# Kernel optimization log

Hardware: AMD Instinct MI355X
Metric: run time of the kernel (lower is better)

## Reference

```python
import jax, jax.numpy as jnp
import numpy as np
import math

IMG, P, C, D, DEPTH, H, MLP, NCLS, B = 224, 16, 3, 768, 12, 12, 3072, 1000, 32
G = IMG // P          # 14 patches per side
N = G * G             # 196 patches
S = N + 1             # 197 tokens (cls + patches)
DK = D // H
PD = P * P * C        # 768 flattened patch dim


def layer_norm(x, g, b, eps=1e-5):
    mu = jnp.mean(x, axis=-1, keepdims=True)
    var = jnp.mean((x - mu) ** 2, axis=-1, keepdims=True)
    return (x - mu) * jax.lax.rsqrt(var + eps) * g + b


def setup_inputs() -> dict:
    key = jax.random.key(0)
    ks = iter(jax.random.split(key, 32))
    nrm = lambda shape, s=0.02: jax.random.normal(next(ks), shape, jnp.float32) * s
    inp = {
        'x': jax.random.normal(next(ks), (B, C, IMG, IMG), jnp.float32),
        'patch_W': nrm((PD, D)), 'patch_b': jnp.zeros((D,)),
        'cls_token': nrm((1, 1, D)), 'pos_embed': nrm((1, S, D)),
        'Wq': nrm((DEPTH, D, D)), 'bq': jnp.zeros((DEPTH, D)),
        'Wk': nrm((DEPTH, D, D)), 'bk': jnp.zeros((DEPTH, D)),
        'Wv': nrm((DEPTH, D, D)), 'bv': jnp.zeros((DEPTH, D)),
        'Wo': nrm((DEPTH, D, D)), 'bo': jnp.zeros((DEPTH, D)),
        'ln1_g': jnp.ones((DEPTH, D)), 'ln1_b': jnp.zeros((DEPTH, D)),
        'ln2_g': jnp.ones((DEPTH, D)), 'ln2_b': jnp.zeros((DEPTH, D)),
        'W1': nrm((DEPTH, D, MLP)), 'b1': jnp.zeros((DEPTH, MLP)),
        'W2': nrm((DEPTH, MLP, D)), 'b2': jnp.zeros((DEPTH, D)),
        'lnp_g': jnp.ones((D,)), 'lnp_b': jnp.zeros((D,)),
        'head_W': nrm((D, NCLS)), 'head_b': jnp.zeros((NCLS,)),
    }
    return inp


def vit_forward(x, patch_W, patch_b, cls_token, pos_embed,
                Wq, bq, Wk, bk, Wv, bv, Wo, bo,
                ln1_g, ln1_b, ln2_g, ln2_b, W1, b1, W2, b2,
                lnp_g, lnp_b, head_W, head_b):
    b = x.shape[0]
    # faithful replication of torch unfold(2).unfold(3).view: (B,C,G,P,G,P)->(B,C,G,G,P,P)->row-major flatten
    patches = x.reshape(b, C, G, P, G, P).transpose(0, 1, 2, 4, 3, 5).reshape(b, N, PD)
    h = patches @ patch_W + patch_b                              # [B,N,D]
    h = jnp.concatenate([jnp.broadcast_to(cls_token, (b, 1, D)), h], axis=1) + pos_embed
    scale = 1.0 / math.sqrt(DK)
    for i in range(DEPTH):
        y = layer_norm(h, ln1_g[i], ln1_b[i])
        q = (y @ Wq[i] + bq[i]).reshape(b, S, H, DK).transpose(0, 2, 1, 3)
        k = (y @ Wk[i] + bk[i]).reshape(b, S, H, DK).transpose(0, 2, 1, 3)
        v = (y @ Wv[i] + bv[i]).reshape(b, S, H, DK).transpose(0, 2, 1, 3)
        attn = jax.nn.softmax(jnp.einsum('bhqd,bhkd->bhqk', q, k) * scale, axis=-1)
        att = jnp.einsum('bhqk,bhkd->bhqd', attn, v).transpose(0, 2, 1, 3).reshape(b, S, D)
        h = h + att @ Wo[i] + bo[i]
        y = layer_norm(h, ln2_g[i], ln2_b[i])
        h = h + jax.nn.gelu(y @ W1[i] + b1[i], approximate=False) @ W2[i] + b2[i]
    h = layer_norm(h, lnp_g, lnp_b)
    return h[:, 0] @ head_W + head_b                              # [B, NCLS]


def reference(x, patch_W, patch_b, cls_token, pos_embed,
              Wq, bq, Wk, bk, Wv, bv, Wo, bo,
              ln1_g, ln1_b, ln2_g, ln2_b, W1, b1, W2, b2,
              lnp_g, lnp_b, head_W, head_b):
    return vit_forward(x, patch_W, patch_b, cls_token, pos_embed,
                       Wq, bq, Wk, bk, Wv, bv, Wo, bo,
                       ln1_g, ln1_b, ln2_g, ln2_b, W1, b1, W2, b2,
                       lnp_g, lnp_b, head_W, head_b)
```

## Files before the change

kernel.cpp:

```cpp
#include <hip/hip_runtime.h>
#include <hip/hip_bf16.h>


typedef __attribute__((ext_vector_type(8))) short short8;
typedef __attribute__((ext_vector_type(4))) float f32x4;
typedef __attribute__((ext_vector_type(4))) unsigned short us4;

#define MFMA16(a, b, c) __builtin_amdgcn_mfma_f32_16x16x32_bf16(a, b, c, 0, 0, 0)

#define BATCH 32
#define SEQ 197
#define SPAD 208
#define DIM 768
#define HEADS 12
#define DKH 64
#define MLPD 3072
#define NCLS 1000
#define NPATCH 196
#define PDIM 768
#define QKVD 2304
#define ROWS (BATCH * SPAD)

static __device__ __forceinline__ unsigned short f2bf(float f) {
    unsigned int u = __builtin_bit_cast(unsigned int, f);
    u += 0x7fffu + ((u >> 16) & 1u);
    return (unsigned short)(u >> 16);
}

__device__ __forceinline__ void gload16(const void* g, void* l) {
    __builtin_amdgcn_global_load_lds(
        (const __attribute__((address_space(1))) void*)g,
        (__attribute__((address_space(3))) void*)l, 16, 0, 0);
}

__global__ __launch_bounds__(256) void patchify(const float* __restrict__ x,
                                                unsigned short* __restrict__ out) {
    int i = blockIdx.x * 256 + threadIdx.x;
    if (i >= BATCH * NPATCH * PDIM) return;
    int b = i / (NPATCH * PDIM);
    int f = i % (NPATCH * PDIM);
    int c = f / 50176, r = f % 50176;
    int gy = r / 3584, r2 = r % 3584;
    int gx = r2 >> 8, r3 = r2 & 255;
    int py = r3 >> 4, px = r3 & 15;
    float v = x[(((size_t)b * 3 + c) * 224 + gy * 16 + py) * 224 + gx * 16 + px];
    out[i] = f2bf(v);
}

__global__ __launch_bounds__(256) void embed_misc(const float* __restrict__ cls,
                                                  const float* __restrict__ pos,
                                                  float* __restrict__ h) {
    int b = blockIdx.x, t = threadIdx.x;
    float* hb = h + (size_t)b * SPAD * DIM;
    for (int d = t; d < DIM; d += 256) hb[d] = cls[d] + pos[d];
    for (int i = t; i < (SPAD - SEQ) * DIM; i += 256) hb[SEQ * DIM + i] = 0.f;
}

__global__ __launch_bounds__(256) void tconv(const float* __restrict__ src,
                                             unsigned short* __restrict__ dst,
                                             int K, int N) {
    __shared__ float tile[32][33];
    int tn = blockIdx.x, tk = blockIdx.y;
    int t = threadIdx.x, r = t >> 3, c4 = (t & 7) << 2;
    float4 v = *reinterpret_cast<const float4*>(&src[(size_t)(tk * 32 + r) * N + tn * 32 + c4]);
    tile[r][c4 + 0] = v.x; tile[r][c4 + 1] = v.y;
    tile[r][c4 + 2] = v.z; tile[r][c4 + 3] = v.w;
    __syncthreads();
    us4 o = { f2bf(tile[c4 + 0][r]), f2bf(tile[c4 + 1][r]),
              f2bf(tile[c4 + 2][r]), f2bf(tile[c4 + 3][r]) };
    *reinterpret_cast<us4*>(&dst[(size_t)(tn * 32 + r) * K + tk * 32 + c4]) = o;
}

__global__ __launch_bounds__(256) void hconv(const float* __restrict__ src,
                                             unsigned short* __restrict__ dst) {
    __shared__ float tile[32][33];
    int tn = blockIdx.x, tk = blockIdx.y;
    int t = threadIdx.x, r = t >> 3, c4 = (t & 7) << 2;
#pragma unroll
    for (int i = 0; i < 4; ++i) {
        int c = tn * 32 + c4 + i;
        tile[r][c4 + i] = (c < NCLS) ? src[(size_t)(tk * 32 + r) * NCLS + c] : 0.f;
    }
    __syncthreads();
    us4 o = { f2bf(tile[c4 + 0][r]), f2bf(tile[c4 + 1][r]),
              f2bf(tile[c4 + 2][r]), f2bf(tile[c4 + 3][r]) };
    *reinterpret_cast<us4*>(&dst[(size_t)(tn * 32 + r) * 768 + tk * 32 + c4]) = o;
}

__global__ __launch_bounds__(256) void wconvert(const float* __restrict__ q,
                                                const float* __restrict__ k,
                                                const float* __restrict__ v,
                                                const float* __restrict__ o,
                                                const float* __restrict__ w1,
                                                const float* __restrict__ w2,
                                                unsigned short* __restrict__ wT) {
    __shared__ float tile[32][33];
    int tb = blockIdx.x;
    const float* src; unsigned short* dst; int K, N;
    if (tb < 2304) {
        K = 768; N = 768;
        int m = tb / 576; tb -= m * 576;
        src = (m == 0) ? q : (m == 1) ? k : (m == 2) ? v : o;
        dst = wT + (m < 3 ? (size_t)m * 589824 : (size_t)1769472);
    } else if (tb < 4608) {
        tb -= 2304; K = 768; N = 3072; src = w1; dst = wT + 2359296;
    } else {
        tb -= 4608; K = 3072; N = 768; src = w2; dst = wT + 4718592;
    }
    int TN = N >> 5;
    int tn = tb % TN, tk = tb / TN;
    int t = threadIdx.x, r = t >> 3, c4 = (t & 7) << 2;
    float4 vv = *reinterpret_cast<const float4*>(&src[(size_t)(tk * 32 + r) * N + tn * 32 + c4]);
    tile[r][c4 + 0] = vv.x; tile[r][c4 + 1] = vv.y;
    tile[r][c4 + 2] = vv.z; tile[r][c4 + 3] = vv.w;
    __syncthreads();
    us4 ov = { f2bf(tile[c4 + 0][r]), f2bf(tile[c4 + 1][r]),
               f2bf(tile[c4 + 2][r]), f2bf(tile[c4 + 3][r]) };
    *reinterpret_cast<us4*>(&dst[(size_t)(tn * 32 + r) * K + tk * 32 + c4]) = ov;
}

__global__ __launch_bounds__(256) void pack_bias(const float* __restrict__ bq,
                                                 const float* __restrict__ bk,
                                                 const float* __restrict__ bv,
                                                 float* __restrict__ dst) {
    int i = blockIdx.x * 256 + threadIdx.x;
    if (i >= 12 * QKVD) return;
    int l = i / QKVD, c = i % QKVD;
    float v = (c < 768) ? bq[l * 768 + c]
            : (c < 1536) ? bk[l * 768 + c - 768]
                         : bv[l * 768 + c - 1536];
    dst[i] = v;
}

#define MM1(MF, J, NF) \
    acc[MF][NF] = MFMA16(af[J][0], bfr[NF][0], acc[MF][NF]); \
    acc[MF][NF] = MFMA16(af[J][1], bfr[NF][1], acc[MF][NF]);
#define MMROW(MF, J) MM1(MF, J, 0) MM1(MF, J, 1) MM1(MF, J, 2) MM1(MF, J, 3)

#define WAITVM(N) \
    __builtin_amdgcn_sched_barrier(0); \
    asm volatile("s_waitcnt vmcnt(" #N ")" ::: "memory"); \
    __builtin_amdgcn_sched_barrier(0);

template <int MODE>
__global__ __launch_bounds__(512, 2) void gemm8p(
    const unsigned short* __restrict__ A, const unsigned short* __restrict__ Bt,
    const float* __restrict__ bias, int N, int K,
    unsigned short* __restrict__ outb) {
    __shared__ unsigned short Ab[2][16384];
    __shared__ unsigned short Bb[2][16384];
    const int tid = threadIdx.x, lane = tid & 63, wid = tid >> 6;
    const int wm = wid >> 2, wn = wid & 3;
    const int lr = lane & 15, lg = lane >> 4;
    const int ric = lane >> 3, sswz = (lane & 7) ^ ric;
    const int row0 = blockIdx.x * 256, col0 = blockIdx.y * 256;
    const char* pA = (const char*)A + ((size_t)(row0 + wid * 8 + ric) * K) * 2 + sswz * 16;
    const char* pB = (const char*)Bt + ((size_t)(col0 + wid * 8 + ric) * K) * 2 + sswz * 16;
    const int NT = K >> 6;

    auto stA = [&](int q, int ks, int b) {
        gload16(pA + ((size_t)q * 64 * K + ks) * 2, (char*)&Ab[b][0] + q * 8192 + wid * 1024);
    };
    auto stB = [&](int q, int ks, int b) {
        gload16(pB + ((size_t)q * 64 * K + ks) * 2, (char*)&Bb[b][0] + q * 8192 + wid * 1024);
    };

    f32x4 acc[8][4];
#pragma unroll
    for (int m = 0; m < 8; ++m)
#pragma unroll
        for (int n = 0; n < 4; ++n) acc[m][n] = (f32x4){0.f, 0.f, 0.f, 0.f};

    stB(0, 0, 0); stB(1, 0, 0); stB(2, 0, 0); stB(3, 0, 0);
    stA(0, 0, 0); stA(2, 0, 0); stA(1, 0, 0); stA(3, 0, 0);
    if (NT > 1) {
        stB(0, 64, 1); stB(1, 64, 1); stB(2, 64, 1); stB(3, 64, 1);
        stA(0, 64, 1); stA(2, 64, 1);
        WAITVM(4)
    } else {
        WAITVM(0)
    }
    __builtin_amdgcn_s_barrier();

    const int rsw = lr & 7;
    for (int s = 0; s < NT; ++s) {
        const int d = s & 1;
        const unsigned short* Ad = &Ab[d][0];
        const unsigned short* Bd = &Bb[d][0];
        const bool p1ok = (s + 1 < NT), p2ok = (s + 2 < NT);
        short8 bfr[4][2], af[2][2];
#pragma unroll
        for (int nf = 0; nf < 4; ++nf)
#pragma unroll
            for (int kk = 0; kk < 2; ++kk)
                bfr[nf][kk] = *reinterpret_cast<const short8*>(
                    &Bd[(wn * 64 + nf * 16 + lr) * 64 + (((kk * 4 + lg) ^ rsw) << 3)]);
#pragma unroll
        for (int j = 0; j < 2; ++j)
#pragma unroll
            for (int kk = 0; kk < 2; ++kk)
                af[j][kk] = *reinterpret_cast<const short8*>(
                    &Ad[(wm * 128 + (0 + j) * 16 + lr) * 64 + (((kk * 4 + lg) ^ rsw) << 3)]);
        if (p1ok) { stA(1, (s + 1) * 64, d ^ 1); stA(3, (s + 1) * 64, d ^ 1); }
        __builtin_amdgcn_s_barrier();
        __builtin_amdgcn_s_setprio(1);
        MMROW(0, 0) MMROW(1, 1)
        __builtin_amdgcn_s_setprio(0);
        __builtin_amdgcn_s_barrier();
#pragma unroll
        for (int j = 0; j < 2; ++j)
#pragma unroll
            for (int kk = 0; kk < 2; ++kk)
                af[j][kk] = *reinterpret_cast<const short8*>(
                    &Ad[(wm * 128 + (2 + j) * 16 + lr) * 64 + (((kk * 4 + lg) ^ rsw) << 3)]);
        if (p2ok) { stB(0, (s + 2) * 64, d); stB(1, (s + 2) * 64, d); }
        __builtin_amdgcn_s_barrier();
        __builtin_amdgcn_s_setprio(1);
        MMROW(2, 0) MMROW(3, 1)
        __builtin_amdgcn_s_setprio(0);
        __builtin_amdgcn_s_barrier();
#pragma unroll
        for (int j = 0; j < 2; ++j)
#pragma unroll
            for (int kk = 0; kk < 2; ++kk)
                af[j][kk] = *reinterpret_cast<const short8*>(
                    &Ad[(wm * 128 + (4 + j) * 16 + lr) * 64 + (((kk * 4 + lg) ^ rsw) << 3)]);
        if (p2ok) { stB(2, (s + 2) * 64, d); stB(3, (s + 2) * 64, d); }
        __builtin_amdgcn_s_barrier();
        __builtin_amdgcn_s_setprio(1);
        MMROW(4, 0) MMROW(5, 1)
        __builtin_amdgcn_s_setprio(0);
        __builtin_amdgcn_s_barrier();
#pragma unroll
        for (int j = 0; j < 2; ++j)
#pragma unroll
            for (int kk = 0; kk < 2; ++kk)
                af[j][kk] = *reinterpret_cast<const short8*>(
                    &Ad[(wm * 128 + (6 + j) * 16 + lr) * 64 + (((kk * 4 + lg) ^ rsw) << 3)]);
        if (p2ok) {
            stA(0, (s + 2) * 64, d); stA(2, (s + 2) * 64, d);
            WAITVM(4)
        } else {
            WAITVM(0)
        }
        __builtin_amdgcn_s_barrier();
        __builtin_amdgcn_s_setprio(1);
        MMROW(6, 0) MMROW(7, 1)
        __builtin_amdgcn_s_setprio(0);
        __builtin_amdgcn_s_barrier();
    }
#pragma unroll
    for (int m = 0; m < 8; ++m) {
#pragma unroll
        for (int n = 0; n < 4; ++n) {
            int gcol = col0 + wn * 64 + n * 16 + lr;
            float bv = bias[gcol];
#pragma unroll
            for (int i = 0; i < 4; ++i) {
                int grow = row0 + wm * 128 + m * 16 + lg * 4 + i;
                float v = acc[m][n][i] + bv;
                if (MODE == 2) v = 0.5f * v * (1.f + erff(v * 0.70710678118654752f));
                outb[(size_t)grow * N + gcol] = f2bf(v);
            }
        }
    }
}

template <int BM>
__global__ __launch_bounds__(256) void gemm_tn(
    const unsigned short* __restrict__ A, const unsigned short* __restrict__ Bt,
    const float* __restrict__ bias, int M, int N, int K, int mode,
    unsigned short* __restrict__ outb, float* __restrict__ outf,
    const float* __restrict__ pos) {
    constexpr int MFRAG = BM / 32;
    constexpr int ACH = BM / 8;
    constexpr int TOT = ACH + 16;
    constexpr int CPW = TOT / 4;
    __shared__ unsigned short Alds[BM * 64];
    __shared__ unsigned short Blds[128 * 64];
    const int tid = threadIdx.x, lane = tid & 63, wid = tid >> 6;
    const int row0 = blockIdx.x * BM, col0 = blockIdx.y * 128;
    const int wm = (wid >> 1) * (BM / 2), wn = (wid & 1) * 64;
    const int lr = lane & 15, lg = lane >> 4;
    const int ric = lane >> 3;
    const int sswz = (lane & 7) ^ ric;

    const char* gptr[CPW];
    char* lptr[CPW];
#pragma unroll
    for (int j = 0; j < CPW; ++j) {
        int cc = wid * CPW + j;
        if (cc < ACH) {
            int grow = row0 + cc * 8 + ric;
            gptr[j] = (const char*)A + (size_t)grow * K * 2 + sswz * 16;
            lptr[j] = (char*)Alds + cc * 1024;
        } else {
            int grow = col0 + (cc - ACH) * 8 + ric;
            gptr[j] = (const char*)Bt + (size_t)grow * K * 2 + sswz * 16;
            lptr[j] = (char*)Blds + (cc - ACH) * 1024;
        }
    }

    f32x4 acc[MFRAG][4];
#pragma unroll
    for (int m = 0; m < MFRAG; ++m)
#pragma unroll
        for (int n = 0; n < 4; ++n) acc[m][n] = (f32x4){0.f, 0.f, 0.f, 0.f};

    const int rsw = lr & 7;
    for (int ks = 0; ks < K; ks += 64) {
        __syncthreads();
#pragma unroll
        for (int j = 0; j < CPW; ++j) {
            gload16(gptr[j], lptr[j]);
            gptr[j] += 128;
        }
        __syncthreads();
        short8 af[MFRAG][2], bfr[4][2];
#pragma unroll
        for (int m = 0; m < MFRAG; ++m)
#pragma unroll
            for (int kk = 0; kk < 2; ++kk)
                af[m][kk] = *reinterpret_cast<const short8*>(
                    &Alds[(wm + m * 16 + lr) * 64 + (((kk * 4 + lg) ^ rsw) << 3)]);
#pragma unroll
        for (int n = 0; n < 4; ++n)
#pragma unroll
            for (int kk = 0; kk < 2; ++kk)
                bfr[n][kk] = *reinterpret_cast<const short8*>(
                    &Blds[(wn + n * 16 + lr) * 64 + (((kk * 4 + lg) ^ rsw) << 3)]);
#pragma unroll
        for (int m = 0; m < MFRAG; ++m)
#pragma unroll
            for (int n = 0; n < 4; ++n) {
                acc[m][n] = MFMA16(af[m][0], bfr[n][0], acc[m][n]);
                acc[m][n] = MFMA16(af[m][1], bfr[n][1], acc[m][n]);
            }
    }
#pragma unroll
    for (int m = 0; m < MFRAG; ++m) {
#pragma unroll
        for (int n = 0; n < 4; ++n) {
            int gcol = col0 + wn + n * 16 + lr;
            float bv = bias ? bias[gcol] : 0.f;
#pragma unroll
            for (int i = 0; i < 4; ++i) {
                int grow = row0 + wm + m * 16 + lg * 4 + i;
                float v = acc[m][n][i] + bv;
                if (mode == 0) {
                    outb[(size_t)grow * N + gcol] = f2bf(v);
                } else if (mode == 1) {
                    outf[(size_t)grow * N + gcol] += v;
                } else if (mode == 2) {
                    v = 0.5f * v * (1.f + erff(v * 0.70710678118654752f));
                    outb[(size_t)grow * N + gcol] = f2bf(v);
                } else if (mode == 3) {
                    int pb = grow / NPATCH, pn = grow % NPATCH;
                    size_t o = ((size_t)pb * SPAD + 1 + pn) * DIM + gcol;
                    outf[o] = v + pos[(size_t)(1 + pn) * DIM + gcol];
                } else {
                    if (grow < BATCH && gcol < NCLS)
                        outf[(size_t)grow * NCLS + gcol] = v + pos[gcol];
                }
            }
        }
    }
}

__global__ __launch_bounds__(256) void ln_bf16(const float* __restrict__ x,
                                               const float* __restrict__ g,
                                               const float* __restrict__ b,
                                               unsigned short* __restrict__ y) {
    __shared__ float red[8];
    int row = blockIdx.x, t = threadIdx.x;
    const float* xr = x + (size_t)row * DIM;
    float v0 = xr[t], v1 = xr[t + 256], v2 = xr[t + 512];
    float s = v0 + v1 + v2, sq = v0 * v0 + v1 * v1 + v2 * v2;
#pragma unroll
    for (int off = 1; off < 64; off <<= 1) {
        s += __shfl_xor(s, off);
        sq += __shfl_xor(sq, off);
    }
    if ((t & 63) == 0) { red[t >> 6] = s; red[4 + (t >> 6)] = sq; }
    __syncthreads();
    s = red[0] + red[1] + red[2] + red[3];
    sq = red[4] + red[5] + red[6] + red[7];
    float mu = s * (1.f / 768.f);
    float var = fmaxf(sq * (1.f / 768.f) - mu * mu, 0.f);
    float rs = rsqrtf(var + 1e-5f);
    unsigned short* yr = y + (size_t)row * DIM;
    yr[t]       = f2bf((v0 - mu) * rs * g[t] + b[t]);
    yr[t + 256] = f2bf((v1 - mu) * rs * g[t + 256] + b[t + 256]);
    yr[t + 512] = f2bf((v2 - mu) * rs * g[t + 512] + b[t + 512]);
}

__global__ __launch_bounds__(256) void ln_cls(const float* __restrict__ x,
                                              const float* __restrict__ g,
                                              const float* __restrict__ b,
                                              unsigned short* __restrict__ y) {
    __shared__ float red[8];
    int bb = blockIdx.x, t = threadIdx.x;
    unsigned short* yr = y + (size_t)bb * DIM;
    if (bb >= BATCH) {
        yr[t] = 0; yr[t + 256] = 0; yr[t + 512] = 0;
        return;
    }
    const float* xr = x + (size_t)bb * SPAD * DIM;
    float v0 = xr[t], v1 = xr[t + 256], v2 = xr[t + 512];
    float s = v0 + v1 + v2, sq = v0 * v0 + v1 * v1 + v2 * v2;
#pragma unroll
    for (int off = 1; off < 64; off <<= 1) {
        s += __shfl_xor(s, off);
        sq += __shfl_xor(sq, off);
    }
    if ((t & 63) == 0) { red[t >> 6] = s; red[4 + (t >> 6)] = sq; }
    __syncthreads();
    s = red[0] + red[1] + red[2] + red[3];
    sq = red[4] + red[5] + red[6] + red[7];
    float mu = s * (1.f / 768.f);
    float var = fmaxf(sq * (1.f / 768.f) - mu * mu, 0.f);
    float rs = rsqrtf(var + 1e-5f);
    yr[t]       = f2bf((v0 - mu) * rs * g[t] + b[t]);
    yr[t + 256] = f2bf((v1 - mu) * rs * g[t + 256] + b[t + 256]);
    yr[t + 512] = f2bf((v2 - mu) * rs * g[t + 512] + b[t + 512]);
}

__global__ __launch_bounds__(256) void attn_fused(const unsigned short* __restrict__ qkv,
                                                  unsigned short* __restrict__ att) {
    __shared__ unsigned short Klds[26 * 512];
    __shared__ unsigned short Vlds[64][232];
    __shared__ unsigned short Plds[4][16 * 256];
    int h = blockIdx.x, b = blockIdx.y, tid = threadIdx.x;
    int wid = tid >> 6, lane = tid & 63, lr = lane & 15, lg = lane >> 4;
    const int ric = lane >> 3, sswz = (lane & 7) ^ ric;

    const char* pK = (const char*)qkv +
        ((size_t)(b * SPAD + ric) * QKVD + 768 + h * DKH) * 2 + sswz * 16;
    for (int c = wid; c < 26; c += 4)
        gload16(pK + (size_t)c * 8 * QKVD * 2, (char*)Klds + c * 1024);

    for (int idx = tid; idx < SPAD * 8; idx += 256) {
        int s = idx >> 3, dc = (idx & 7) << 3;
        uint4 w = *reinterpret_cast<const uint4*>(
            &qkv[((size_t)b * SPAD + s) * QKVD + 1536 + h * DKH + dc]);
        const unsigned short* pe = reinterpret_cast<const unsigned short*>(&w);
#pragma unroll
        for (int i = 0; i < 8; ++i) Vlds[dc + i][s] = pe[i];
    }
    for (int i = tid; i < 64 * 24; i += 256) Vlds[i / 24][208 + (i % 24)] = 0;
    __syncthreads();

    unsigned short* Pw = &Plds[wid][0];
    const short8 zero8 = {0, 0, 0, 0, 0, 0, 0, 0};
    const int rowin = lr & 7;

    for (int qt = wid; qt < 13; qt += 4) {
        size_t qoff = ((size_t)b * SPAD + qt * 16 + lr) * QKVD + h * DKH + lg * 8;
        short8 qf0 = *reinterpret_cast<const short8*>(&qkv[qoff]);
        short8 qf1 = *reinterpret_cast<const short8*>(&qkv[qoff + 32]);
        f32x4 acc[13];
#pragma unroll
        for (int kt = 0; kt < 13; ++kt) {
            const unsigned short* kbase = Klds + (kt * 2 + (lr >> 3)) * 512 + rowin * 64;
            short8 kf0 = *reinterpret_cast<const short8*>(&kbase[(lg ^ rowin) << 3]);
            short8 kf1 = *reinterpret_cast<const short8*>(&kbase[((4 + lg) ^ rowin) << 3]);
            f32x4 a = (f32x4){0.f, 0.f, 0.f, 0.f};
            a = MFMA16(qf0, kf0, a);
            a = MFMA16(qf1, kf1, a);
            acc[kt] = a;
        }
#pragma unroll
        for (int kt = 0; kt < 13; ++kt)
#pragma unroll
            for (int r = 0; r < 4; ++r) acc[kt][r] *= 0.125f;
        if (lr >= 5) {
#pragma unroll
            for (int r = 0; r < 4; ++r) acc[12][r] = -1e30f;
        }
        float mx[4] = {-1e30f, -1e30f, -1e30f, -1e30f};
#pragma unroll
        for (int kt = 0; kt < 13; ++kt)
#pragma unroll
            for (int r = 0; r < 4; ++r) mx[r] = fmaxf(mx[r], acc[kt][r]);
#pragma unroll
        for (int r = 0; r < 4; ++r) {
            mx[r] = fmaxf(mx[r], __shfl_xor(mx[r], 1));
            mx[r] = fmaxf(mx[r], __shfl_xor(mx[r], 2));
            mx[r] = fmaxf(mx[r], __shfl_xor(mx[r], 4));
            mx[r] = fmaxf(mx[r], __shfl_xor(mx[r], 8));
        }
        float sm[4] = {0.f, 0.f, 0.f, 0.f};
#pragma unroll
        for (int kt = 0; kt < 13; ++kt)
#pragma unroll
            for (int r = 0; r < 4; ++r) {
                float e = __expf(acc[kt][r] - mx[r]);
                acc[kt][r] = e;
                sm[r] += e;
            }
#pragma unroll
        for (int r = 0; r < 4; ++r) {
            sm[r] += __shfl_xor(sm[r], 1);
            sm[r] += __shfl_xor(sm[r], 2);
            sm[r] += __shfl_xor(sm[r], 4);
            sm[r] += __shfl_xor(sm[r], 8);
        }
#pragma unroll
        for (int r = 0; r < 4; ++r) {
            int row = lg * 4 + r;
            float inv = 1.f / sm[r];
#pragma unroll
            for (int kt = 0; kt < 13; ++kt) {
                int col = kt * 16 + lr;
                int idx = row * 256 + ((((col >> 3) ^ (row & 7)) << 3) | (col & 7));
                Pw[idx] = f2bf(acc[kt][r] * inv);
            }
        }
        if (lr < 6) {
            int s = 26 + lr;
#pragma unroll
            for (int r = 0; r < 4; ++r) {
                int row = lg * 4 + r;
                *reinterpret_cast<short8*>(&Pw[row * 256 + ((s ^ (row & 7)) << 3)]) = zero8;
            }
        }
        int rsw = lr & 7;
#pragma unroll
        for (int dt = 0; dt < 4; ++dt) {
            f32x4 a = (f32x4){0.f, 0.f, 0.f, 0.f};
#pragma unroll
            for (int kk = 0; kk < 7; ++kk) {
                short8 af = *reinterpret_cast<const short8*>(
                    &Pw[lr * 256 + (((kk * 4 + lg) ^ rsw) << 3)]);
                short8 bfr = *reinterpret_cast<const short8*>(
                    &Vlds[dt * 16 + lr][kk * 32 + lg * 8]);
                a = MFMA16(af, bfr, a);
            }
#pragma unroll
            for (int i = 0; i < 4; ++i) {
                int s = qt * 16 + lg * 4 + i;
                att[((size_t)b * SPAD + s) * DIM + h * DKH + dt * 16 + lr] = f2bf(a[i]);
            }
        }
    }
}

extern "C" void kernel_launch(void* const* d_in, const int* in_sizes, int n_in,
                              void* d_out, int out_size, void* d_ws, size_t ws_size,
                              hipStream_t stream) {
    const float* x      = (const float*)d_in[0];
    const float* patchW = (const float*)d_in[1];
    const float* patchB = (const float*)d_in[2];
    const float* clstok = (const float*)d_in[3];
    const float* pose   = (const float*)d_in[4];
    const float* Wq = (const float*)d_in[5];
    const float* bq = (const float*)d_in[6];
    const float* Wk = (const float*)d_in[7];
    const float* bk = (const float*)d_in[8];
    const float* Wv = (const float*)d_in[9];
    const float* bv = (const float*)d_in[10];
    const float* Wo = (const float*)d_in[11];
    const float* bo = (const float*)d_in[12];
    const float* ln1g = (const float*)d_in[13];
    const float* ln1b = (const float*)d_in[14];
    const float* ln2g = (const float*)d_in[15];
    const float* ln2b = (const float*)d_in[16];
    const float* W1 = (const float*)d_in[17];
    const float* b1 = (const float*)d_in[18];
    const float* W2 = (const float*)d_in[19];
    const float* b2 = (const float*)d_in[20];
    const float* lnpg = (const float*)d_in[21];
    const float* lnpb = (const float*)d_in[22];
    const float* headW = (const float*)d_in[23];
    const float* headB = (const float*)d_in[24];
    float* out = (float*)d_out;

    constexpr size_t SZ_H   = (size_t)ROWS * DIM * 4;
    constexpr size_t SZ_QKV = (size_t)ROWS * QKVD * 2;
    constexpr size_t SZ_Y   = (size_t)ROWS * DIM * 2;
    constexpr size_t SZ_M1  = (size_t)ROWS * MLPD * 2;
    constexpr size_t SZ_WT  = (size_t)7077888 * 2;
    char* w = (char*)d_ws;
    float* hbuf            = (float*)w;
    unsigned short* qkvb   = (unsigned short*)(w + SZ_H);
    unsigned short* ybuf   = (unsigned short*)(w + SZ_H + SZ_QKV);
    unsigned short* m1buf  = (unsigned short*)(w + SZ_H + SZ_QKV + SZ_Y);
    unsigned short* wT     = (unsigned short*)(w + SZ_H + SZ_QKV + SZ_Y + SZ_M1);
    float* bqkv            = (float*)(w + SZ_H + SZ_QKV + SZ_Y + SZ_M1 + SZ_WT);
    unsigned short* patches = m1buf;
    unsigned short* clsbuf  = m1buf;
    unsigned short* hwT     = m1buf + 64 * DIM;

    pack_bias<<<dim3(108), 256, 0, stream>>>(bq, bk, bv, bqkv);

    tconv<<<dim3(24, 24), 256, 0, stream>>>(patchW, wT, PDIM, DIM);
    patchify<<<dim3((BATCH * NPATCH * PDIM + 255) / 256), 256, 0, stream>>>(x, patches);
    embed_misc<<<dim3(BATCH), 256, 0, stream>>>(clstok, pose, hbuf);
    gemm_tn<64><<<dim3(98, 6), 256, 0, stream>>>(patches, wT, patchB,
                                                 BATCH * NPATCH, DIM, PDIM, 3,
                                                 nullptr, hbuf, pose);

    for (int i = 0; i < 12; ++i) {
        const size_t wo = (size_t)i * DIM * DIM;
        const size_t wm = (size_t)i * DIM * MLPD;
        wconvert<<<dim3(6912), 256, 0, stream>>>(Wq + wo, Wk + wo, Wv + wo, Wo + wo,
                                                 W1 + wm, W2 + wm, wT);
        ln_bf16<<<dim3(ROWS), 256, 0, stream>>>(hbuf, ln1g + i * DIM, ln1b + i * DIM, ybuf);
        gemm8p<0><<<dim3(26, 9), 512, 0, stream>>>(ybuf, wT, bqkv + i * QKVD,
                                                   QKVD, DIM, qkvb);
        attn_fused<<<dim3(HEADS, BATCH), 256, 0, stream>>>(qkvb, ybuf);
        gemm_tn<64><<<dim3(104, 6), 256, 0, stream>>>(ybuf, wT + 1769472, bo + i * DIM,
                                                      ROWS, DIM, DIM, 1,
                                                      nullptr, hbuf, nullptr);
        ln_bf16<<<dim3(ROWS), 256, 0, stream>>>(hbuf, ln2g + i * DIM, ln2b + i * DIM, ybuf);
        gemm8p<2><<<dim3(26, 12), 512, 0, stream>>>(ybuf, wT + 2359296, b1 + i * MLPD,
                                                    MLPD, DIM, m1buf);
        gemm_tn<64><<<dim3(104, 6), 256, 0, stream>>>(m1buf, wT + 4718592, b2 + i * DIM,
                                                      ROWS, DIM, MLPD, 1,
                                                      nullptr, hbuf, nullptr);
    }
    ln_cls<<<dim3(64), 256, 0, stream>>>(hbuf, lnpg, lnpb, clsbuf);
    hconv<<<dim3(32, 24), 256, 0, stream>>>(headW, hwT);
    gemm_tn<64><<<dim3(1, 8), 256, 0, stream>>>(clsbuf, hwT, nullptr,
                                                64, 1024, DIM, 4,
                                                nullptr, out, headB);
}
```

Baseline: 3.044 ms.

## Convert all layer weights in one launch and switch MLP1 to gemm_tn<128>

Result: slower. 3.292 ms (+8.1%).

```diff
diff --git a/kernel.cpp b/kernel.cpp
--- a/kernel.cpp
+++ b/kernel.cpp
@@ -20,6 +20,7 @@
 #define PDIM 768
 #define QKVD 2304
 #define ROWS (BATCH * SPAD)
+#define WT_ELEMS 7077888
 
 static __device__ __forceinline__ unsigned short f2bf(float f) {
     unsigned int u = __builtin_bit_cast(unsigned int, f);
@@ -87,15 +88,23 @@
     *reinterpret_cast<us4*>(&dst[(size_t)(tn * 32 + r) * 768 + tk * 32 + c4]) = o;
 }
 
-__global__ __launch_bounds__(256) void wconvert(const float* __restrict__ q,
-                                                const float* __restrict__ k,
-                                                const float* __restrict__ v,
-                                                const float* __restrict__ o,
-                                                const float* __restrict__ w1,
-                                                const float* __restrict__ w2,
-                                                unsigned short* __restrict__ wT) {
+__global__ __launch_bounds__(256) void wconvert(const float* __restrict__ q0,
+                                                const float* __restrict__ k0,
+                                                const float* __restrict__ v0,
+                                                const float* __restrict__ o0,
+                                                const float* __restrict__ w10,
+                                                const float* __restrict__ w20,
+                                                unsigned short* __restrict__ wT0) {
     __shared__ float tile[32][33];
-    int tb = blockIdx.x;
+    int layer = blockIdx.x / 6912;
+    int tb = blockIdx.x % 6912;
+    const float* q  = q0  + (size_t)layer * DIM * DIM;
+    const float* k  = k0  + (size_t)layer * DIM * DIM;
+    const float* v  = v0  + (size_t)layer * DIM * DIM;
+    const float* o  = o0  + (size_t)layer * DIM * DIM;
+    const float* w1 = w10 + (size_t)layer * DIM * MLPD;
+    const float* w2 = w20 + (size_t)layer * DIM * MLPD;
+    unsigned short* wT = wT0 + (size_t)layer * WT_ELEMS;
     const float* src; unsigned short* dst; int K, N;
     if (tb < 2304) {
         K = 768; N = 768;
@@ -579,43 +588,54 @@
     constexpr size_t SZ_QKV = (size_t)ROWS * QKVD * 2;
     constexpr size_t SZ_Y   = (size_t)ROWS * DIM * 2;
     constexpr size_t SZ_M1  = (size_t)ROWS * MLPD * 2;
-    constexpr size_t SZ_WT  = (size_t)7077888 * 2;
+    constexpr size_t SZ_WT  = (size_t)WT_ELEMS * 2;
+    constexpr size_t SZ_BQ  = (size_t)12 * QKVD * 4;
+    const size_t base = SZ_H + SZ_QKV + SZ_Y + SZ_M1;
+    const bool big = ws_size >= base + 12 * SZ_WT + SZ_BQ;
+    const int nwt = big ? 12 : 1;
+
     char* w = (char*)d_ws;
     float* hbuf            = (float*)w;
     unsigned short* qkvb   = (unsigned short*)(w + SZ_H);
     unsigned short* ybuf   = (unsigned short*)(w + SZ_H + SZ_QKV);
     unsigned short* m1buf  = (unsigned short*)(w + SZ_H + SZ_QKV + SZ_Y);
-    unsigned short* wT     = (unsigned short*)(w + SZ_H + SZ_QKV + SZ_Y + SZ_M1);
-    float* bqkv            = (float*)(w + SZ_H + SZ_QKV + SZ_Y + SZ_M1 + SZ_WT);
+    unsigned short* wT     = (unsigned short*)(w + base);
+    float* bqkv            = (float*)(w + base + (size_t)nwt * SZ_WT);
     unsigned short* patches = m1buf;
+    unsigned short* pwT     = ybuf;
     unsigned short* clsbuf  = m1buf;
     unsigned short* hwT     = m1buf + 64 * DIM;
 
     pack_bias<<<dim3(108), 256, 0, stream>>>(bq, bk, bv, bqkv);
-
-    tconv<<<dim3(24, 24), 256, 0, stream>>>(patchW, wT, PDIM, DIM);
+    if (big)
+        wconvert<<<dim3(12 * 6912), 256, 0, stream>>>(Wq, Wk, Wv, Wo, W1, W2, wT);
+
+    tconv<<<dim3(24, 24), 256, 0, stream>>>(patchW, pwT, PDIM, DIM);
     patchify<<<dim3((BATCH * NPATCH * PDIM + 255) / 256), 256, 0, stream>>>(x, patches);
     embed_misc<<<dim3(BATCH), 256, 0, stream>>>(clstok, pose, hbuf);
-    gemm_tn<64><<<dim3(98, 6), 256, 0, stream>>>(patches, wT, patchB,
+    gemm_tn<64><<<dim3(98, 6), 256, 0, stream>>>(patches, pwT, patchB,
                                                  BATCH * NPATCH, DIM, PDIM, 3,
                                                  nullptr, hbuf, pose);
 
     for (int i = 0; i < 12; ++i) {
-        const size_t wo = (size_t)i * DIM * DIM;
-        const size_t wm = (size_t)i * DIM * MLPD;
-        wconvert<<<dim3(6912), 256, 0, stream>>>(Wq + wo, Wk + wo, Wv + wo, Wo + wo,
-                                                 W1 + wm, W2 + wm, wT);
+        unsigned short* wTl = wT + (size_t)(big ? i : 0) * WT_ELEMS;
+        if (!big)
+            wconvert<<<dim3(6912), 256, 0, stream>>>(
+                Wq + (size_t)i * DIM * DIM, Wk + (size_t)i * DIM * DIM,
+                Wv + (size_t)i * DIM * DIM, Wo + (size_t)i * DIM * DIM,
+                W1 + (size_t)i * DIM * MLPD, W2 + (size_t)i * DIM * MLPD, wTl);
         ln_bf16<<<dim3(ROWS), 256, 0, stream>>>(hbuf, ln1g + i * DIM, ln1b + i * DIM, ybuf);
-        gemm8p<0><<<dim3(26, 9), 512, 0, stream>>>(ybuf, wT, bqkv + i * QKVD,
+        gemm8p<0><<<dim3(26, 9), 512, 0, stream>>>(ybuf, wTl, bqkv + i * QKVD,
                                                    QKVD, DIM, qkvb);
         attn_fused<<<dim3(HEADS, BATCH), 256, 0, stream>>>(qkvb, ybuf);
-        gemm_tn<64><<<dim3(104, 6), 256, 0, stream>>>(ybuf, wT + 1769472, bo + i * DIM,
+        gemm_tn<64><<<dim3(104, 6), 256, 0, stream>>>(ybuf, wTl + 1769472, bo + i * DIM,
                                                       ROWS, DIM, DIM, 1,
                                                       nullptr, hbuf, nullptr);
         ln_bf16<<<dim3(ROWS), 256, 0, stream>>>(hbuf, ln2g + i * DIM, ln2b + i * DIM, ybuf);
-        gemm8p<2><<<dim3(26, 12), 512, 0, stream>>>(ybuf, wT + 2359296, b1 + i * MLPD,
-                                                    MLPD, DIM, m1buf);
-        gemm_tn<64><<<dim3(104, 6), 256, 0, stream>>>(m1buf, wT + 4718592, b2 + i * DIM,
+        gemm_tn<128><<<dim3(52, 24), 256, 0, stream>>>(ybuf, wTl + 2359296, b1 + i * MLPD,
+                                                       ROWS, MLPD, DIM, 2,
+                                                       m1buf, nullptr, nullptr);
+        gemm_tn<64><<<dim3(104, 6), 256, 0, stream>>>(m1buf, wTl + 4718592, b2 + i * DIM,
                                                       ROWS, DIM, MLPD, 1,
                                                       nullptr, hbuf, nullptr);
     }
```
